# Kernel tuning notes

Measured on AMD Instinct MI355X. Metric: run time of the kernel, lower is better.

## Reference

```python
import jax, jax.numpy as jnp
import numpy as np

EPS = 1e-5
M = 8          # num_modules
NUM_LAYERS = 4


def gumbel_softmax(logits, u, tau):
    g = -jnp.log(-jnp.log(jnp.clip(u, 1e-10, 1.0 - 1e-7)))
    return jax.nn.softmax((logits + g) / tau, axis=-1)


def batchnorm(x, gamma, beta):
    # training-mode BN over batch axis 0; x: [B, ...], gamma/beta broadcast over trailing dims
    mean = jnp.mean(x, axis=0, keepdims=True)
    var = jnp.mean(jnp.square(x - mean), axis=0, keepdims=True)  # biased var, as torch BN
    return (x - mean) * jax.lax.rsqrt(var + EPS) * gamma + beta


def setup_inputs() -> dict:
    key = jax.random.key(0)
    ks = jax.random.split(key, 32)
    B = 16384
    d = {}
    d['x'] = jax.random.normal(ks[0], (B, 128), jnp.float32)
    d['embedding_input'] = jax.random.normal(ks[1], (B, 128), jnp.float32)
    d['u_sel'] = jax.random.uniform(ks[2], (B, NUM_LAYERS - 1, M, M), jnp.float32)
    d['u_final'] = jax.random.uniform(ks[3], (B, M), jnp.float32)
    shapes = [('base_W0', (128, 400)), ('base_b0', (400,)), ('base_W1', (400, 256)), ('base_b1', (256,)),
              ('em_W0', (128, 400)), ('em_b0', (400,)),
              ('gat_W0', (400, 256)), ('gat_b0', (256,)), ('gat_W1', (256, 256)), ('gat_b1', (256,)),
              ('sel_W', (3, 256, 64)), ('sel_b', (3, 64)), ('selF_W', (256, 8)), ('selF_b', (8,)),
              ('cond_W', (3, 64, 256)), ('cond_b', (3, 256)),
              ('mod_W', (8, 256, 256)), ('mod_b', (8, 256)),
              ('last_W', (256, 18)), ('last_b', (18,))]
    for i, (name, sh) in enumerate(shapes):
        fan_in = sh[-2] if len(sh) >= 2 else sh[-1]
        d[name] = jax.random.normal(ks[4 + i], sh, jnp.float32) / np.sqrt(fan_in)
    d['bn1_g'] = jnp.ones((8, 256), jnp.float32)
    d['bn1_b'] = jnp.zeros((8, 256), jnp.float32)
    d['bn2_g'] = jnp.ones((8, 256), jnp.float32)
    d['bn2_b'] = jnp.zeros((8, 256), jnp.float32)
    return d


def forward(x, embedding_input, u_sel, u_final,
            base_W0, base_b0, base_W1, base_b1, em_W0, em_b0,
            gat_W0, gat_b0, gat_W1, gat_b1,
            sel_W, sel_b, selF_W, selF_b, cond_W, cond_b,
            mod_W, mod_b, bn1_g, bn1_b, bn2_g, bn2_b, last_W, last_b):
    relu = jax.nn.relu
    # base MLP (last activation is identity)
    h = relu(x @ base_W0 + base_b0)
    out = h @ base_W1 + base_b1                       # [B, 256]
    # embedding base (single layer, identity last activation)
    emb = embedding_input @ em_W0 + em_b0             # [B, 400]
    # gating fcs: activation THEN fc, per source loop
    emb = relu(emb) @ gat_W0 + gat_b0
    emb = relu(emb) @ gat_W1 + gat_b1                 # [B, 256]

    # routing logits (stochastic branch, tau = select_temp = 1.0)
    select_input = relu(emb)
    gsels = []
    for i in range(NUM_LAYERS - 1):
        logit = jnp.tanh(select_input @ sel_W[i] + sel_b[i])       # [B, 64]
        sraw = logit.reshape(logit.shape[0], M, M)                  # [B, M, M]
        gsels.append(gumbel_softmax(sraw, u_sel[:, i], 1.0))
        select_input = relu((logit @ cond_W[i] + cond_b[i]) * emb)
    final_select = gumbel_softmax(select_input @ selF_W + selF_b, u_final, 1.0)  # [B, M]
    # selects were insert(0, ...)'d in torch -> consumed in reversed order
    selects = gsels[::-1]

    # layer-0 expert modules: BN -> Linear -> BN (only layers[0] is used in forward)
    mean = jnp.mean(out, axis=0, keepdims=True)
    var = jnp.mean(jnp.square(out - mean), axis=0, keepdims=True)
    xhat = (out - mean) * jax.lax.rsqrt(var + EPS)                  # shared normalization
    t = xhat[:, None, :] * bn1_g + bn1_b                            # [B, M, 256] per-module affine
    h = jnp.einsum('bmd,mdh->bmh', t, mod_W) + mod_b                # [B, M, 256]
    prev = batchnorm(h, bn2_g, bn2_b)                               # [B, M, 256]

    # cascade: weighted combination + relu per layer
    for l in range(NUM_LAYERS - 1):
        prev = relu(jnp.einsum('bmk,bkh->bmh', selects[l], prev))
    out = jnp.einsum('bm,bmh->bh', final_select, prev)              # [B, 256]
    return out @ last_W + last_b                                    # [B, 18]


def reference(x, embedding_input, u_sel, u_final,
              base_W0, base_b0, base_W1, base_b1, em_W0, em_b0,
              gat_W0, gat_b0, gat_W1, gat_b1,
              sel_W, sel_b, selF_W, selF_b, cond_W, cond_b,
              mod_W, mod_b, bn1_g, bn1_b, bn2_g, bn2_b, last_W, last_b):
    return forward(x, embedding_input, u_sel, u_final,
                   base_W0, base_b0, base_W1, base_b1, em_W0, em_b0,
                   gat_W0, gat_b0, gat_W1, gat_b1,
                   sel_W, sel_b, selF_W, selF_b, cond_W, cond_b,
                   mod_W, mod_b, bn1_g, bn1_b, bn2_g, bn2_b, last_W, last_b)
```

## Files before the change

### kernel.cpp

```cpp
#include <hip/hip_runtime.h>
#include <math.h>


#define EPI_NONE  0
#define EPI_RELU  1
#define EPI_TANH  2
#define EPI_COND  3
#define EPI_STATS 4

typedef short bf16x8 __attribute__((ext_vector_type(8)));
typedef float f32x4 __attribute__((ext_vector_type(4)));

__device__ __forceinline__ unsigned short f2bf(float f) {
  unsigned u = __float_as_uint(f);
  u += 0x7fffu + ((u >> 16) & 1u);
  return (unsigned short)(u >> 16);
}
__device__ __forceinline__ float bf2f(unsigned short h) {
  return __uint_as_float(((unsigned)h) << 16);
}
__device__ __forceinline__ void gload_lds16(const void* g, void* l) {
  __builtin_amdgcn_global_load_lds(
      (const __attribute__((address_space(1))) unsigned int*)g,
      (__attribute__((address_space(3))) unsigned int*)l, 16, 0, 0);
}
__device__ __forceinline__ bf16x8 relu_bf8(bf16x8 v) {
  bf16x8 r;
  #pragma unroll
  for (int j = 0; j < 8; ++j) r[j] = v[j] > 0 ? v[j] : (short)0;
  return r;
}

__global__ __launch_bounds__(256) void prep_all(
    const float* __restrict__ x, const float* __restrict__ embi,
    const float* __restrict__ base_W0, const float* __restrict__ em_W0,
    const float* __restrict__ base_W1, const float* __restrict__ gat_W0,
    const float* __restrict__ gat_W1, const float* __restrict__ sel_W,
    const float* __restrict__ cond_W, const float* __restrict__ last_W,
    unsigned short* __restrict__ x_bf, unsigned short* __restrict__ e_bf,
    unsigned short* __restrict__ W0t, unsigned short* __restrict__ emW0t,
    unsigned short* __restrict__ W1t, unsigned short* __restrict__ g0t,
    unsigned short* __restrict__ g1t, unsigned short* __restrict__ selWt,
    unsigned short* __restrict__ condWt, unsigned short* __restrict__ lastWt,
    float* __restrict__ stats)
{
  __shared__ float t[32][33];
  int bid = blockIdx.x;
  const int tid = threadIdx.x;

  if (bid < 4096) {
    const float* src = bid < 2048 ? x : embi;
    unsigned short* dst = bid < 2048 ? x_bf : e_bf;
    const int i = ((bid & 2047) * 256 + tid) * 4;
    const float4 v = *reinterpret_cast<const float4*>(&src[i]);
    ushort4 o;
    o.x = f2bf(v.x); o.y = f2bf(v.y); o.z = f2bf(v.z); o.w = f2bf(v.w);
    *reinterpret_cast<ushort4*>(&dst[i]) = o;
    return;
  }
  bid -= 4096;

  const int tx = tid & 31, ty = tid >> 5;

  if (bid < 496) {
    const float* src; unsigned short* dst; int K, N, KP, gx, local;
    if (bid < 64)       { src = base_W0; dst = W0t;   K = 128; N = 400; KP = 128; gx = 4;  local = bid; }
    else if (bid < 128) { src = em_W0;   dst = emW0t; K = 128; N = 400; KP = 128; gx = 4;  local = bid - 64; }
    else if (bid < 232) { src = base_W1; dst = W1t;   K = 400; N = 256; KP = 416; gx = 13; local = bid - 128; }
    else if (bid < 336) { src = gat_W0;  dst = g0t;   K = 400; N = 256; KP = 416; gx = 13; local = bid - 232; }
    else if (bid < 400) { src = gat_W1;  dst = g1t;   K = 256; N = 256; KP = 256; gx = 8;  local = bid - 336; }
    else if (bid < 448) {
      const int i = (bid - 400) / 16;
      src = sel_W + i * 16384; dst = selWt + i * 16384;
      K = 256; N = 64; KP = 256; gx = 8; local = (bid - 400) % 16;
    } else {
      const int i = (bid - 448) / 16;
      src = cond_W + i * 16384; dst = condWt + i * 16384;
      K = 64; N = 256; KP = 64; gx = 2; local = (bid - 448) % 16;
    }
    const int k0 = (local % gx) * 32, n0 = (local / gx) * 32;
    #pragma unroll
    for (int p = 0; p < 4; ++p) {
      const int k = k0 + ty + p * 8;
      t[ty + p * 8][tx] = (k < K && n0 + tx < N) ? src[(size_t)k * N + n0 + tx] : 0.f;
    }
    __syncthreads();
    #pragma unroll
    for (int p = 0; p < 4; ++p) {
      const int n = n0 + ty + p * 8;
      dst[(size_t)n * KP + k0 + tx] = f2bf(t[tx][ty + p * 8]);
    }
    return;
  }
  bid -= 496;

  if (bid < 8) {
    const int k0 = bid * 32;
    #pragma unroll
    for (int p = 0; p < 4; ++p)
      t[ty + p * 8][tx] = (tx < 18) ? last_W[(size_t)(k0 + ty + p * 8) * 18 + tx] : 0.f;
    __syncthreads();
    #pragma unroll
    for (int p = 0; p < 4; ++p) {
      const int n = ty + p * 8;
      lastWt[(size_t)n * 256 + k0 + tx] = f2bf(t[tx][n]);
      lastWt[(size_t)(n + 32) * 256 + k0 + tx] = 0;
    }
    return;
  }

  for (int i = tid; i < 4608; i += 256) stats[i] = 0.f;
}

template<int BN, int WM, int WN, int EPI, bool RELU_A>
__global__ __launch_bounds__(256) void gemm_bf16(
    const unsigned short* __restrict__ A, int AS,
    const unsigned short* __restrict__ Wt, const float* __restrict__ bias,
    unsigned short* __restrict__ C, int CS, int Nreal, int NP, int K,
    const unsigned short* __restrict__ emb,
    float* __restrict__ sum, float* __restrict__ sumsq,
    const unsigned short* A2, const unsigned short* W2,
    const float* bias_b, unsigned short* C2)
{
  constexpr int FRAG_M = 128 / WM / 16;
  constexpr int FRAG_N = BN / WN / 16;
  __shared__ unsigned short As[128 * 32];
  __shared__ unsigned short Bs[BN * 32];
  const unsigned short* Ap = (blockIdx.z == 0) ? A : A2;
  const unsigned short* Wp = (blockIdx.z == 0) ? Wt : W2;
  const float* bp = (blockIdx.z == 0) ? bias : bias_b;
  unsigned short* Cp = (blockIdx.z == 0) ? C : C2;
  const int row0 = blockIdx.y * 128;
  const int n0 = blockIdx.x * BN;
  const int tid = threadIdx.x;
  const int wid = tid >> 6, lane = tid & 63;
  const int wr = wid / WN, wc = wid % WN;
  const int arow = tid >> 2;
  const int kcol = (tid & 3) * 8;
  const int lr = lane & 15, lk = (lane >> 4) * 8;
  const int lrow = (lane >> 4) * 4;

  f32x4 acc[FRAG_M][FRAG_N] = {};
  for (int k0 = 0; k0 < K; k0 += 32) {
    gload_lds16(Ap + (size_t)(row0 + arow) * AS + k0 + kcol, (char*)As + tid * 16);
    gload_lds16(Ap + (size_t)(row0 + 64 + arow) * AS + k0 + kcol, (char*)As + 4096 + tid * 16);
    gload_lds16(Wp + (size_t)(n0 + arow) * K + k0 + kcol, (char*)Bs + tid * 16);
    if constexpr (BN == 128)
      gload_lds16(Wp + (size_t)(n0 + 64 + arow) * K + k0 + kcol, (char*)Bs + 4096 + tid * 16);
    __syncthreads();
    bf16x8 a[FRAG_M], b[FRAG_N];
    #pragma unroll
    for (int i = 0; i < FRAG_M; ++i) {
      a[i] = *reinterpret_cast<const bf16x8*>(&As[(wr * (128 / WM) + i * 16 + lr) * 32 + lk]);
      if (RELU_A) a[i] = relu_bf8(a[i]);
    }
    #pragma unroll
    for (int j = 0; j < FRAG_N; ++j)
      b[j] = *reinterpret_cast<const bf16x8*>(&Bs[(wc * (BN / WN) + j * 16 + lr) * 32 + lk]);
    #pragma unroll
    for (int i = 0; i < FRAG_M; ++i)
      #pragma unroll
      for (int j = 0; j < FRAG_N; ++j)
        acc[i][j] = __builtin_amdgcn_mfma_f32_16x16x32_bf16(a[i], b[j], acc[i][j], 0, 0, 0);
    __syncthreads();
  }
  #pragma unroll
  for (int j = 0; j < FRAG_N; ++j) {
    const int col = n0 + wc * (BN / WN) + j * 16 + lr;
    if (col >= NP) continue;
    const bool real = col < Nreal;
    const float bv = real ? bp[col] : 0.f;
    float s = 0.f, q = 0.f;
    #pragma unroll
    for (int i = 0; i < FRAG_M; ++i) {
      #pragma unroll
      for (int r = 0; r < 4; ++r) {
        const int row = row0 + wr * (128 / WM) + i * 16 + lrow + r;
        float v = acc[i][j][r] + bv;
        if (EPI == EPI_RELU) v = fmaxf(v, 0.f);
        if (EPI == EPI_TANH) v = tanhf(v);
        if (EPI == EPI_COND) { v *= bf2f(emb[(size_t)row * 256 + col]); v = fmaxf(v, 0.f); }
        if (!real) v = 0.f;
        const unsigned short hv = f2bf(v);
        Cp[(size_t)row * CS + col] = hv;
        if (EPI == EPI_STATS) {
          const float vr = bf2f(hv);
          s += vr;
          q = fmaf(vr, vr, q);
        }
      }
    }
    if (EPI == EPI_STATS) {
      s += __shfl_xor(s, 16); s += __shfl_xor(s, 32);
      q += __shfl_xor(q, 16); q += __shfl_xor(q, 32);
      if (lane < 16) {
        atomicAdd(&sum[col], s);
        atomicAdd(&sumsq[col], q);
      }
    }
  }
}

__global__ __launch_bounds__(256) void gemm_mod_frag(
    const unsigned short* __restrict__ Abf,
    const unsigned short* __restrict__ Wt2,
    const float* __restrict__ bias2,
    unsigned short* __restrict__ H,
    float* __restrict__ sum, float* __restrict__ sumsq)
{
  __shared__ unsigned short Cs[128 * 136];
  const int tid = threadIdx.x;
  const int wid = tid >> 6, lane = tid & 63;
  const int wr = wid >> 1, wc = wid & 1;
  const int lr = lane & 15, hi = lane >> 4;
  const int m = blockIdx.x >> 1, half = blockIdx.x & 1;
  const int row0 = blockIdx.y * 128;

  const unsigned short* Wbase =
      Wt2 + (size_t)(m * 16 + half * 8 + wc * 4) * 8 * 512 + lane * 8;
  const unsigned short* Abase = Abf + (size_t)(row0 + wr * 64 + lr) * 256 + hi * 8;

  f32x4 acc[4][4] = {};
  #pragma unroll 2
  for (int ks = 0; ks < 8; ++ks) {
    bf16x8 a[4], b[4];
    #pragma unroll
    for (int i = 0; i < 4; ++i)
      a[i] = *reinterpret_cast<const bf16x8*>(Abase + (size_t)i * 16 * 256 + ks * 32);
    #pragma unroll
    for (int j = 0; j < 4; ++j)
      b[j] = *reinterpret_cast<const bf16x8*>(Wbase + ((size_t)j * 8 + ks) * 512);
    #pragma unroll
    for (int i = 0; i < 4; ++i)
      #pragma unroll
      for (int j = 0; j < 4; ++j)
        acc[i][j] = __builtin_amdgcn_mfma_f32_16x16x32_bf16(a[i], b[j], acc[i][j], 0, 0, 0);
  }

  #pragma unroll
  for (int j = 0; j < 4; ++j) {
    const int J = half * 8 + wc * 4 + j;
    const int gc = m * 256 + J * 16 + lr;
    const float bv = bias2[gc];
    float s = 0.f, q = 0.f;
    #pragma unroll
    for (int i = 0; i < 4; ++i) {
      #pragma unroll
      for (int r = 0; r < 4; ++r) {
        const unsigned short hv = f2bf(acc[i][j][r] + bv);
        Cs[(wr * 64 + i * 16 + hi * 4 + r) * 136 + wc * 64 + j * 16 + lr] = hv;
        const float vr = bf2f(hv);
        s += vr;
        q = fmaf(vr, vr, q);
      }
    }
    s += __shfl_xor(s, 16); s += __shfl_xor(s, 32);
    q += __shfl_xor(q, 16); q += __shfl_xor(q, 32);
    if (lane < 16) {
      atomicAdd(&sum[gc], s);
      atomicAdd(&sumsq[gc], q);
    }
  }
  __syncthreads();
  const int colbase = m * 256 + half * 128;
  #pragma unroll
  for (int pass = 0; pass < 2; ++pass) {
    const int row = pass * 64 + (tid >> 2);
    const int qc = (tid & 3) * 32;
    #pragma unroll
    for (int v = 0; v < 4; ++v) {
      const uint4 d = *reinterpret_cast<const uint4*>(&Cs[row * 136 + qc + v * 8]);
      *reinterpret_cast<uint4*>(&H[(size_t)(row0 + row) * 2048 + colbase + qc + v * 8]) = d;
    }
  }
}

__global__ void gumbel8(const unsigned short* __restrict__ logit, const float* __restrict__ u,
                        float* __restrict__ out, int u_off, int u_stride)
{
  const int idx = blockIdx.x * 256 + threadIdx.x;
  const int b = idx >> 3, m = idx & 7;
  const unsigned short* lp = logit + (size_t)b * 64 + m * 8;
  const float* up = u + (size_t)b * u_stride + u_off + m * 8;
  float v[8];
  #pragma unroll
  for (int j = 0; j < 8; ++j) {
    const float uu = fminf(fmaxf(up[j], 1e-10f), 0.9999999f);
    v[j] = bf2f(lp[j]) - logf(-logf(uu));
  }
  float mx = v[0];
  #pragma unroll
  for (int j = 1; j < 8; ++j) mx = fmaxf(mx, v[j]);
  float s = 0.f;
  #pragma unroll
  for (int j = 0; j < 8; ++j) { v[j] = expf(v[j] - mx); s += v[j]; }
  const float inv = 1.f / s;
  float* op = out + (size_t)b * 64 + m * 8;
  #pragma unroll
  for (int j = 0; j < 8; ++j) op[j] = v[j] * inv;
}

__global__ void final_select_k(const unsigned short* __restrict__ si, const float* __restrict__ Wf,
                               const float* __restrict__ bias, const float* __restrict__ u,
                               float* __restrict__ fs)
{
  const int idx = blockIdx.x * 256 + threadIdx.x;
  const int b = idx >> 3, j = idx & 7;
  const unsigned short* sp = si + (size_t)b * 256;
  float acc = bias[j];
  for (int k = 0; k < 256; ++k) acc = fmaf(bf2f(sp[k]), Wf[k * 8 + j], acc);
  const float uu = fminf(fmaxf(u[(size_t)b * 8 + j], 1e-10f), 0.9999999f);
  float v = acc - logf(-logf(uu));
  float mx = v;
  #pragma unroll
  for (int d = 1; d < 8; d <<= 1) mx = fmaxf(mx, __shfl_xor(mx, d, 8));
  float e = expf(v - mx);
  float s = e;
  #pragma unroll
  for (int d = 1; d < 8; d <<= 1) s += __shfl_xor(s, d, 8);
  fs[(size_t)b * 8 + j] = e / s;
}

__global__ __launch_bounds__(256) void fold_modw_all(
    const float* __restrict__ W, const float* __restrict__ g1,
    const float* __restrict__ b1, const float* __restrict__ modb,
    const float* __restrict__ sum1, const float* __restrict__ sumsq1,
    unsigned short* __restrict__ Wt, float* __restrict__ bias2)
{
  const float invB = 1.f / 16384.f;
  if (blockIdx.z == 8) {
    if (blockIdx.y != 0) return;
    const int m = blockIdx.x, h = threadIdx.x;
    float acc = modb[m * 256 + h];
    for (int d = 0; d < 256; ++d) {
      const float mean = sum1[d] * invB;
      const float var = sumsq1[d] * invB - mean * mean;
      const float r = rsqrtf(var + 1e-5f);
      const float c = b1[m * 256 + d] - mean * r * g1[m * 256 + d];
      acc = fmaf(c, W[((size_t)m * 256 + d) * 256 + h], acc);
    }
    bias2[m * 256 + h] = acc;
    return;
  }
  __shared__ float t[32][33];
  const int m = blockIdx.z, d0 = blockIdx.y * 32, h0 = blockIdx.x * 32;
  const int tx = threadIdx.x & 31, ty = threadIdx.x >> 5;
  #pragma unroll
  for (int p = 0; p < 4; ++p) {
    const int d = d0 + ty + p * 8;
    const float mean = sum1[d] * invB;
    const float var = sumsq1[d] * invB - mean * mean;
    const float r = rsqrtf(var + 1e-5f);
    t[ty + p * 8][tx] = W[((size_t)m * 256 + d) * 256 + h0 + tx] * r * g1[m * 256 + d];
  }
  __syncthreads();
  #pragma unroll
  for (int p = 0; p < 4; ++p) {
    const int h = h0 + ty + p * 8;
    Wt[((size_t)m * 256 + h) * 256 + d0 + tx] = f2bf(t[tx][ty + p * 8]);
  }
}

__global__ __launch_bounds__(256) void reshuffle_w(
    const unsigned short* __restrict__ modWt, unsigned short* __restrict__ Wt2)
{
  const int idx = blockIdx.x * 256 + threadIdx.x;
  const int ks = idx & 7, col = (idx >> 3) & 255, m = idx >> 11;
  const unsigned short* src = modWt + ((size_t)m * 256 + col) * 256 + ks * 32;
  unsigned short* dst = Wt2 + (size_t)((m * 16 + (col >> 4)) * 8 + ks) * 512 + (col & 15) * 8;
  #pragma unroll
  for (int h2 = 0; h2 < 4; ++h2)
    *reinterpret_cast<uint4*>(dst + h2 * 128) = *reinterpret_cast<const uint4*>(src + h2 * 8);
}

__global__ void finalize_bn2(const float* __restrict__ sum, const float* __restrict__ sumsq,
                             const float* __restrict__ g, const float* __restrict__ b,
                             float* __restrict__ scale, float* __restrict__ shift)
{
  const int i = blockIdx.x * 256 + threadIdx.x;
  const float invB = 1.f / 16384.f;
  const float m = sum[i] * invB;
  const float v = sumsq[i] * invB - m * m;
  const float r = rsqrtf(v + 1e-5f);
  const float sc = r * g[i];
  scale[i] = sc;
  shift[i] = b[i] - m * sc;
}

__global__ __launch_bounds__(256) void final_cascade(
    const unsigned short* __restrict__ H, const float* __restrict__ scale2,
    const float* __restrict__ shift2, const float* __restrict__ gs0,
    const float* __restrict__ gs1, const float* __restrict__ gs2,
    const float* __restrict__ fs, unsigned short* __restrict__ ovec)
{
  const int wave = threadIdx.x >> 6, lane = threadIdx.x & 63;
  const int b = __builtin_amdgcn_readfirstlane(blockIdx.x * 4 + wave);
  const int c0 = lane << 2;

  float prev[8][4];
  #pragma unroll
  for (int m = 0; m < 8; ++m) {
    const int gc = m * 256 + c0;
    const ushort4 h = *reinterpret_cast<const ushort4*>(&H[(size_t)b * 2048 + gc]);
    const float4 sc = *reinterpret_cast<const float4*>(&scale2[gc]);
    const float4 sh = *reinterpret_cast<const float4*>(&shift2[gc]);
    prev[m][0] = bf2f(h.x) * sc.x + sh.x;
    prev[m][1] = bf2f(h.y) * sc.y + sh.y;
    prev[m][2] = bf2f(h.z) * sc.z + sh.z;
    prev[m][3] = bf2f(h.w) * sc.w + sh.w;
  }

  const float* sel0 = gs2 + (size_t)b * 64;
  const float* sel1 = gs1 + (size_t)b * 64;
  const float* sel2 = gs0 + (size_t)b * 64;
  #pragma unroll
  for (int l = 0; l < 3; ++l) {
    const float* sp = (l == 0) ? sel0 : (l == 1) ? sel1 : sel2;
    float nw[8][4];
    #pragma unroll
    for (int m = 0; m < 8; ++m) {
      float a0 = 0.f, a1 = 0.f, a2 = 0.f, a3 = 0.f;
      #pragma unroll
      for (int k = 0; k < 8; ++k) {
        const float s = sp[m * 8 + k];
        a0 = fmaf(s, prev[k][0], a0);
        a1 = fmaf(s, prev[k][1], a1);
        a2 = fmaf(s, prev[k][2], a2);
        a3 = fmaf(s, prev[k][3], a3);
      }
      nw[m][0] = fmaxf(a0, 0.f); nw[m][1] = fmaxf(a1, 0.f);
      nw[m][2] = fmaxf(a2, 0.f); nw[m][3] = fmaxf(a3, 0.f);
    }
    #pragma unroll
    for (int m = 0; m < 8; ++m)
      #pragma unroll
      for (int c = 0; c < 4; ++c)
        prev[m][c] = nw[m][c];
  }

  const float* fp = fs + (size_t)b * 8;
  float ov[4] = {0.f, 0.f, 0.f, 0.f};
  #pragma unroll
  for (int m = 0; m < 8; ++m) {
    const float s = fp[m];
    ov[0] = fmaf(s, prev[m][0], ov[0]);
    ov[1] = fmaf(s, prev[m][1], ov[1]);
    ov[2] = fmaf(s, prev[m][2], ov[2]);
    ov[3] = fmaf(s, prev[m][3], ov[3]);
  }
  ushort4 o;
  o.x = f2bf(ov[0]); o.y = f2bf(ov[1]); o.z = f2bf(ov[2]); o.w = f2bf(ov[3]);
  *reinterpret_cast<ushort4*>(&ovec[(size_t)b * 256 + c0]) = o;
}

__global__ __launch_bounds__(256) void gemm_last(
    const unsigned short* __restrict__ A, const unsigned short* __restrict__ Wt,
    const float* __restrict__ bias, float* __restrict__ out)
{
  __shared__ unsigned short As[128 * 32];
  __shared__ unsigned short Bs[64 * 32];
  const int row0 = blockIdx.y * 128;
  const int tid = threadIdx.x;
  const int wid = tid >> 6, lane = tid & 63;
  const int arow = tid >> 2;
  const int kcol = (tid & 3) * 8;
  const int lr = lane & 15, lk = (lane >> 4) * 8;
  const int lrow = (lane >> 4) * 4;

  f32x4 acc[2][4] = {};
  for (int k0 = 0; k0 < 256; k0 += 32) {
    gload_lds16(A + (size_t)(row0 + arow) * 256 + k0 + kcol, (char*)As + tid * 16);
    gload_lds16(A + (size_t)(row0 + 64 + arow) * 256 + k0 + kcol, (char*)As + 4096 + tid * 16);
    gload_lds16(Wt + (size_t)arow * 256 + k0 + kcol, (char*)Bs + tid * 16);
    __syncthreads();
    bf16x8 a[2], b[4];
    #pragma unroll
    for (int i = 0; i < 2; ++i)
      a[i] = *reinterpret_cast<const bf16x8*>(&As[(wid * 32 + i * 16 + lr) * 32 + lk]);
    #pragma unroll
    for (int j = 0; j < 4; ++j)
      b[j] = *reinterpret_cast<const bf16x8*>(&Bs[(j * 16 + lr) * 32 + lk]);
    #pragma unroll
    for (int i = 0; i < 2; ++i)
      #pragma unroll
      for (int j = 0; j < 4; ++j)
        acc[i][j] = __builtin_amdgcn_mfma_f32_16x16x32_bf16(a[i], b[j], acc[i][j], 0, 0, 0);
    __syncthreads();
  }
  #pragma unroll
  for (int j = 0; j < 2; ++j) {
    const int col = j * 16 + lr;
    if (col >= 18) continue;
    const float bv = bias[col];
    #pragma unroll
    for (int i = 0; i < 2; ++i) {
      #pragma unroll
      for (int r = 0; r < 4; ++r) {
        const int row = row0 + wid * 32 + i * 16 + lrow + r;
        out[(size_t)row * 18 + col] = acc[i][j][r] + bv;
      }
    }
  }
}

extern "C" void kernel_launch(void* const* d_in, const int* in_sizes, int n_in,
                              void* d_out, int out_size, void* d_ws, size_t ws_size,
                              hipStream_t stream)
{
  (void)in_sizes; (void)n_in; (void)out_size; (void)ws_size;
  const float* x       = (const float*)d_in[0];
  const float* embi    = (const float*)d_in[1];
  const float* u_sel   = (const float*)d_in[2];
  const float* u_fin   = (const float*)d_in[3];
  const float* base_W0 = (const float*)d_in[4];
  const float* base_b0 = (const float*)d_in[5];
  const float* base_W1 = (const float*)d_in[6];
  const float* base_b1 = (const float*)d_in[7];
  const float* em_W0   = (const float*)d_in[8];
  const float* em_b0   = (const float*)d_in[9];
  const float* gat_W0  = (const float*)d_in[10];
  const float* gat_b0  = (const float*)d_in[11];
  const float* gat_W1  = (const float*)d_in[12];
  const float* gat_b1  = (const float*)d_in[13];
  const float* sel_W   = (const float*)d_in[14];
  const float* sel_b   = (const float*)d_in[15];
  const float* selF_W  = (const float*)d_in[16];
  const float* selF_b  = (const float*)d_in[17];
  const float* cond_W  = (const float*)d_in[18];
  const float* cond_b  = (const float*)d_in[19];
  const float* mod_W   = (const float*)d_in[20];
  const float* mod_b   = (const float*)d_in[21];
  const float* last_W  = (const float*)d_in[22];
  const float* last_b  = (const float*)d_in[23];
  const float* bn1_g   = (const float*)d_in[24];
  const float* bn1_b   = (const float*)d_in[25];
  const float* bn2_g   = (const float*)d_in[26];
  const float* bn2_b   = (const float*)d_in[27];

  char* WSB = (char*)d_ws;
  unsigned short* h_big    = (unsigned short*)(WSB + 0);
  unsigned short* h1e      = (unsigned short*)(WSB + 67108864);
  unsigned short* ovec_bf  = (unsigned short*)(WSB + 67108864);
  unsigned short* h1       = (unsigned short*)(WSB + 81000448);
  unsigned short* x_bf     = (unsigned short*)(WSB + 94631936);
  unsigned short* e_bf     = (unsigned short*)(WSB + 98826240);
  unsigned short* emb_bf   = (unsigned short*)(WSB + 103020544);
  unsigned short* si_bf    = (unsigned short*)(WSB + 111409152);
  unsigned short* out_bf   = (unsigned short*)(WSB + 119797760);
  unsigned short* logit_bf = (unsigned short*)(WSB + 128186368);
  float* gs0   = (float*)(WSB + 130283520);
  float* gs1   = (float*)(WSB + 134477824);
  float* gs2   = (float*)(WSB + 138672128);
  float* bufFs = (float*)(WSB + 142866432);
  unsigned short* W0t   = (unsigned short*)(WSB + 143390720);
  unsigned short* emW0t = (unsigned short*)(WSB + 143521792);
  unsigned short* W1t   = (unsigned short*)(WSB + 143652864);
  unsigned short* g0t   = (unsigned short*)(WSB + 143865856);
  unsigned short* g1t   = (unsigned short*)(WSB + 144078848);
  unsigned short* selWt = (unsigned short*)(WSB + 144209920);
  unsigned short* condWt= (unsigned short*)(WSB + 144308224);
  unsigned short* modWt = (unsigned short*)(WSB + 144406528);
  unsigned short* Wt2   = (unsigned short*)(WSB + 145455104);
  float* bias2  = (float*)(WSB + 146503680);
  float* stats  = (float*)(WSB + 146511872);
  unsigned short* lastWt = (unsigned short*)(WSB + 146530304);
  float* scale2 = (float*)(WSB + 146563072);
  float* shift2 = (float*)(WSB + 146571264);
  float* sum1   = stats;        float* sumsq1 = stats + 256;
  float* sum2   = stats + 512;  float* sumsq2 = stats + 2560;

  const dim3 blk(256);
  prep_all<<<dim3(4601), blk, 0, stream>>>(
      x, embi, base_W0, em_W0, base_W1, gat_W0, gat_W1, sel_W, cond_W, last_W,
      x_bf, e_bf, W0t, emW0t, W1t, g0t, g1t, selWt, condWt, lastWt, stats);

  gemm_bf16<128, 2, 2, EPI_RELU, false><<<dim3(4, 128, 2), blk, 0, stream>>>(
      x_bf, 128, W0t, base_b0, h1, 416, 400, 416, 128, nullptr, nullptr, nullptr,
      e_bf, emW0t, em_b0, h1e);
  gemm_bf16<64, 4, 1, EPI_STATS, false><<<dim3(4, 128), blk, 0, stream>>>(
      h1, 416, W1t, base_b1, out_bf, 256, 256, 256, 416, nullptr, sum1, sumsq1,
      nullptr, nullptr, nullptr, nullptr);
  gemm_bf16<64, 4, 1, EPI_RELU, false><<<dim3(4, 128), blk, 0, stream>>>(
      h1e, 416, g0t, gat_b0, si_bf, 256, 256, 256, 416, nullptr, nullptr, nullptr,
      nullptr, nullptr, nullptr, nullptr);
  gemm_bf16<64, 4, 1, EPI_NONE, false><<<dim3(4, 128), blk, 0, stream>>>(
      si_bf, 256, g1t, gat_b1, emb_bf, 256, 256, 256, 256, nullptr, nullptr, nullptr,
      nullptr, nullptr, nullptr, nullptr);
  float* gs[3] = {gs0, gs1, gs2};
  for (int i = 0; i < 3; ++i) {
    if (i == 0)
      gemm_bf16<64, 4, 1, EPI_TANH, true><<<dim3(1, 128), blk, 0, stream>>>(
          emb_bf, 256, selWt, sel_b, logit_bf, 64, 64, 64, 256, nullptr, nullptr, nullptr,
          nullptr, nullptr, nullptr, nullptr);
    else
      gemm_bf16<64, 4, 1, EPI_TANH, false><<<dim3(1, 128), blk, 0, stream>>>(
          si_bf, 256, selWt + i * 16384, sel_b + i * 64, logit_bf, 64, 64, 64, 256,
          nullptr, nullptr, nullptr, nullptr, nullptr, nullptr, nullptr);
    gumbel8<<<dim3(512), blk, 0, stream>>>(logit_bf, u_sel, gs[i], i * 64, 192);
    gemm_bf16<64, 4, 1, EPI_COND, false><<<dim3(4, 128), blk, 0, stream>>>(
        logit_bf, 64, condWt + i * 16384, cond_b + i * 256, si_bf, 256, 256, 256, 64,
        emb_bf, nullptr, nullptr, nullptr, nullptr, nullptr, nullptr);
  }
  final_select_k<<<dim3(512), blk, 0, stream>>>(si_bf, selF_W, selF_b, u_fin, bufFs);
  fold_modw_all<<<dim3(8, 8, 9), blk, 0, stream>>>(
      mod_W, bn1_g, bn1_b, mod_b, sum1, sumsq1, modWt, bias2);
  reshuffle_w<<<dim3(64), blk, 0, stream>>>(modWt, Wt2);
  gemm_mod_frag<<<dim3(16, 128), blk, 0, stream>>>(
      out_bf, Wt2, bias2, h_big, sum2, sumsq2);
  finalize_bn2<<<dim3(8), blk, 0, stream>>>(sum2, sumsq2, bn2_g, bn2_b, scale2, shift2);
  final_cascade<<<dim3(4096), blk, 0, stream>>>(
      h_big, scale2, shift2, gs0, gs1, gs2, bufFs, ovec_bf);
  gemm_last<<<dim3(1, 128), blk, 0, stream>>>(ovec_bf, lastWt, last_b, (float*)d_out);
}
```

Measured before the change: 288.9 us.

## Fuse input conversion into first GEMM, fuse select pipeline, replace mod GEMM

The first GEMM now reads the fp32 inputs directly and converts them to bf16 while staging into LDS, so the separate conversion pass and its intermediate buffers are gone. Each selection layer's logits GEMM, tanh, Gumbel-softmax and conditioning GEMM are merged into one kernel that keeps the logits in LDS, replacing three launches per layer. The fragment-layout module GEMM and its weight reshuffle kernel are replaced by a plain LDS-tiled GEMM with a swizzled block order and direct global stores. The risks are that the fused select kernel runs only 128 blocks with a heavy per-block workload, and that the new module GEMM may perform worse than the pre-reshuffled direct-load version.

```diff
diff --git a/kernel.cpp b/kernel.cpp
--- a/kernel.cpp
+++ b/kernel.cpp
@@ -1,12 +1,6 @@
 #include <hip/hip_runtime.h>
 #include <math.h>
 
-
-#define EPI_NONE  0
-#define EPI_RELU  1
-#define EPI_TANH  2
-#define EPI_COND  3
-#define EPI_STATS 4
 
 typedef short bf16x8 __attribute__((ext_vector_type(8)));
 typedef float f32x4 __attribute__((ext_vector_type(4)));
@@ -19,6 +13,9 @@
 __device__ __forceinline__ float bf2f(unsigned short h) {
   return __uint_as_float(((unsigned)h) << 16);
 }
+__device__ __forceinline__ unsigned pack2(float a, float b) {
+  return ((unsigned)f2bf(b) << 16) | f2bf(a);
+}
 __device__ __forceinline__ void gload_lds16(const void* g, void* l) {
   __builtin_amdgcn_global_load_lds(
       (const __attribute__((address_space(1))) unsigned int*)g,
@@ -31,13 +28,15 @@
   return r;
 }
 
+#define EPI_NONE  0
+#define EPI_RELU  1
+#define EPI_STATS 4
+
 __global__ __launch_bounds__(256) void prep_all(
-    const float* __restrict__ x, const float* __restrict__ embi,
     const float* __restrict__ base_W0, const float* __restrict__ em_W0,
     const float* __restrict__ base_W1, const float* __restrict__ gat_W0,
     const float* __restrict__ gat_W1, const float* __restrict__ sel_W,
     const float* __restrict__ cond_W, const float* __restrict__ last_W,
-    unsigned short* __restrict__ x_bf, unsigned short* __restrict__ e_bf,
     unsigned short* __restrict__ W0t, unsigned short* __restrict__ emW0t,
     unsigned short* __restrict__ W1t, unsigned short* __restrict__ g0t,
     unsigned short* __restrict__ g1t, unsigned short* __restrict__ selWt,
@@ -47,19 +46,6 @@
   __shared__ float t[32][33];
   int bid = blockIdx.x;
   const int tid = threadIdx.x;
-
-  if (bid < 4096) {
-    const float* src = bid < 2048 ? x : embi;
-    unsigned short* dst = bid < 2048 ? x_bf : e_bf;
-    const int i = ((bid & 2047) * 256 + tid) * 4;
-    const float4 v = *reinterpret_cast<const float4*>(&src[i]);
-    ushort4 o;
-    o.x = f2bf(v.x); o.y = f2bf(v.y); o.z = f2bf(v.z); o.w = f2bf(v.w);
-    *reinterpret_cast<ushort4*>(&dst[i]) = o;
-    return;
-  }
-  bid -= 4096;
-
   const int tx = tid & 31, ty = tid >> 5;
 
   if (bid < 496) {
@@ -112,24 +98,89 @@
   for (int i = tid; i < 4608; i += 256) stats[i] = 0.f;
 }
 
+__global__ __launch_bounds__(256) void gemm_w0(
+    const float* __restrict__ Ax, const float* __restrict__ Ae,
+    const unsigned short* __restrict__ Wx, const unsigned short* __restrict__ We,
+    const float* __restrict__ bx, const float* __restrict__ be,
+    unsigned short* __restrict__ Cx, unsigned short* __restrict__ Ce)
+{
+  __shared__ unsigned short As[128 * 32];
+  __shared__ unsigned short Bs[128 * 32];
+  const float* Ap = blockIdx.z ? Ae : Ax;
+  const unsigned short* Wp = blockIdx.z ? We : Wx;
+  const float* bp = blockIdx.z ? be : bx;
+  unsigned short* Cp = blockIdx.z ? Ce : Cx;
+  const int row0 = blockIdx.y * 128;
+  const int n0 = blockIdx.x * 128;
+  const int tid = threadIdx.x;
+  const int wid = tid >> 6, lane = tid & 63;
+  const int wr = wid >> 1, wc = wid & 1;
+  const int arow = tid >> 2, kcol = (tid & 3) * 8;
+  const int lr = lane & 15, lk = (lane >> 4) * 8;
+  const int lrow = (lane >> 4) * 4;
+
+  f32x4 acc[4][4] = {};
+  for (int k0 = 0; k0 < 128; k0 += 32) {
+    {
+      const float4* s1 = reinterpret_cast<const float4*>(
+          Ap + (size_t)(row0 + arow) * 128 + k0 + kcol);
+      uint4 w1 = {pack2(s1[0].x, s1[0].y), pack2(s1[0].z, s1[0].w),
+                  pack2(s1[1].x, s1[1].y), pack2(s1[1].z, s1[1].w)};
+      *reinterpret_cast<uint4*>(&As[arow * 32 + kcol]) = w1;
+      const float4* s2 = reinterpret_cast<const float4*>(
+          Ap + (size_t)(row0 + 64 + arow) * 128 + k0 + kcol);
+      uint4 w2 = {pack2(s2[0].x, s2[0].y), pack2(s2[0].z, s2[0].w),
+                  pack2(s2[1].x, s2[1].y), pack2(s2[1].z, s2[1].w)};
+      *reinterpret_cast<uint4*>(&As[(64 + arow) * 32 + kcol]) = w2;
+    }
+    gload_lds16(Wp + (size_t)(n0 + arow) * 128 + k0 + kcol, (char*)Bs + tid * 16);
+    gload_lds16(Wp + (size_t)(n0 + 64 + arow) * 128 + k0 + kcol,
+                (char*)Bs + 4096 + tid * 16);
+    __syncthreads();
+    bf16x8 a[4], b[4];
+    #pragma unroll
+    for (int i = 0; i < 4; ++i)
+      a[i] = *reinterpret_cast<const bf16x8*>(&As[(wr * 64 + i * 16 + lr) * 32 + lk]);
+    #pragma unroll
+    for (int j = 0; j < 4; ++j)
+      b[j] = *reinterpret_cast<const bf16x8*>(&Bs[(wc * 64 + j * 16 + lr) * 32 + lk]);
+    #pragma unroll
+    for (int i = 0; i < 4; ++i)
+      #pragma unroll
+      for (int j = 0; j < 4; ++j)
+        acc[i][j] = __builtin_amdgcn_mfma_f32_16x16x32_bf16(a[i], b[j], acc[i][j], 0, 0, 0);
+    __syncthreads();
+  }
+  #pragma unroll
+  for (int j = 0; j < 4; ++j) {
+    const int col = n0 + wc * 64 + j * 16 + lr;
+    if (col >= 416) continue;
+    const bool real = col < 400;
+    const float bv = real ? bp[col] : 0.f;
+    #pragma unroll
+    for (int i = 0; i < 4; ++i) {
+      #pragma unroll
+      for (int r = 0; r < 4; ++r) {
+        const int row = row0 + wr * 64 + i * 16 + lrow + r;
+        float v = real ? fmaxf(acc[i][j][r] + bv, 0.f) : 0.f;
+        Cp[(size_t)row * 416 + col] = f2bf(v);
+      }
+    }
+  }
+}
+
 template<int BN, int WM, int WN, int EPI, bool RELU_A>
 __global__ __launch_bounds__(256) void gemm_bf16(
     const unsigned short* __restrict__ A, int AS,
     const unsigned short* __restrict__ Wt, const float* __restrict__ bias,
     unsigned short* __restrict__ C, int CS, int Nreal, int NP, int K,
     const unsigned short* __restrict__ emb,
-    float* __restrict__ sum, float* __restrict__ sumsq,
-    const unsigned short* A2, const unsigned short* W2,
-    const float* bias_b, unsigned short* C2)
+    float* __restrict__ sum, float* __restrict__ sumsq)
 {
   constexpr int FRAG_M = 128 / WM / 16;
   constexpr int FRAG_N = BN / WN / 16;
   __shared__ unsigned short As[128 * 32];
   __shared__ unsigned short Bs[BN * 32];
-  const unsigned short* Ap = (blockIdx.z == 0) ? A : A2;
-  const unsigned short* Wp = (blockIdx.z == 0) ? Wt : W2;
-  const float* bp = (blockIdx.z == 0) ? bias : bias_b;
-  unsigned short* Cp = (blockIdx.z == 0) ? C : C2;
   const int row0 = blockIdx.y * 128;
   const int n0 = blockIdx.x * BN;
   const int tid = threadIdx.x;
@@ -142,11 +193,11 @@
 
   f32x4 acc[FRAG_M][FRAG_N] = {};
   for (int k0 = 0; k0 < K; k0 += 32) {
-    gload_lds16(Ap + (size_t)(row0 + arow) * AS + k0 + kcol, (char*)As + tid * 16);
-    gload_lds16(Ap + (size_t)(row0 + 64 + arow) * AS + k0 + kcol, (char*)As + 4096 + tid * 16);
-    gload_lds16(Wp + (size_t)(n0 + arow) * K + k0 + kcol, (char*)Bs + tid * 16);
+    gload_lds16(A + (size_t)(row0 + arow) * AS + k0 + kcol, (char*)As + tid * 16);
+    gload_lds16(A + (size_t)(row0 + 64 + arow) * AS + k0 + kcol, (char*)As + 4096 + tid * 16);
+    gload_lds16(Wt + (size_t)(n0 + arow) * K + k0 + kcol, (char*)Bs + tid * 16);
     if constexpr (BN == 128)
-      gload_lds16(Wp + (size_t)(n0 + 64 + arow) * K + k0 + kcol, (char*)Bs + 4096 + tid * 16);
+      gload_lds16(Wt + (size_t)(n0 + 64 + arow) * K + k0 + kcol, (char*)Bs + 4096 + tid * 16);
     __syncthreads();
     bf16x8 a[FRAG_M], b[FRAG_N];
     #pragma unroll
@@ -169,7 +220,7 @@
     const int col = n0 + wc * (BN / WN) + j * 16 + lr;
     if (col >= NP) continue;
     const bool real = col < Nreal;
-    const float bv = real ? bp[col] : 0.f;
+    const float bv = real ? bias[col] : 0.f;
     float s = 0.f, q = 0.f;
     #pragma unroll
     for (int i = 0; i < FRAG_M; ++i) {
@@ -178,11 +229,9 @@
         const int row = row0 + wr * (128 / WM) + i * 16 + lrow + r;
         float v = acc[i][j][r] + bv;
         if (EPI == EPI_RELU) v = fmaxf(v, 0.f);
-        if (EPI == EPI_TANH) v = tanhf(v);
-        if (EPI == EPI_COND) { v *= bf2f(emb[(size_t)row * 256 + col]); v = fmaxf(v, 0.f); }
         if (!real) v = 0.f;
         const unsigned short hv = f2bf(v);
-        Cp[(size_t)row * CS + col] = hv;
+        C[(size_t)row * CS + col] = hv;
         if (EPI == EPI_STATS) {
           const float vr = bf2f(hv);
           s += vr;
@@ -201,54 +250,59 @@
   }
 }
 
-__global__ __launch_bounds__(256) void gemm_mod_frag(
-    const unsigned short* __restrict__ Abf,
-    const unsigned short* __restrict__ Wt2,
-    const float* __restrict__ bias2,
-    unsigned short* __restrict__ H,
+__global__ __launch_bounds__(256) void gemm_mod(
+    const unsigned short* __restrict__ A,
+    const unsigned short* __restrict__ Wt,
+    const float* __restrict__ bias, unsigned short* __restrict__ C,
     float* __restrict__ sum, float* __restrict__ sumsq)
 {
-  __shared__ unsigned short Cs[128 * 136];
+  __shared__ unsigned short As[128 * 32];
+  __shared__ unsigned short Bs[128 * 32];
+  const int lin = blockIdx.x;
+  const int swz = (lin & 7) * 256 + (lin >> 3);
+  const int row0 = (swz >> 4) * 128;
+  const int n0 = (swz & 15) * 128;
   const int tid = threadIdx.x;
   const int wid = tid >> 6, lane = tid & 63;
   const int wr = wid >> 1, wc = wid & 1;
-  const int lr = lane & 15, hi = lane >> 4;
-  const int m = blockIdx.x >> 1, half = blockIdx.x & 1;
-  const int row0 = blockIdx.y * 128;
-
-  const unsigned short* Wbase =
-      Wt2 + (size_t)(m * 16 + half * 8 + wc * 4) * 8 * 512 + lane * 8;
-  const unsigned short* Abase = Abf + (size_t)(row0 + wr * 64 + lr) * 256 + hi * 8;
+  const int arow = tid >> 2;
+  const int kcol = (tid & 3) * 8;
+  const int lr = lane & 15, lk = (lane >> 4) * 8;
+  const int lrow = (lane >> 4) * 4;
 
   f32x4 acc[4][4] = {};
-  #pragma unroll 2
-  for (int ks = 0; ks < 8; ++ks) {
+  for (int k0 = 0; k0 < 256; k0 += 32) {
+    gload_lds16(A + (size_t)(row0 + arow) * 256 + k0 + kcol, (char*)As + tid * 16);
+    gload_lds16(A + (size_t)(row0 + 64 + arow) * 256 + k0 + kcol, (char*)As + 4096 + tid * 16);
+    gload_lds16(Wt + (size_t)(n0 + arow) * 256 + k0 + kcol, (char*)Bs + tid * 16);
+    gload_lds16(Wt + (size_t)(n0 + 64 + arow) * 256 + k0 + kcol, (char*)Bs + 4096 + tid * 16);
+    __syncthreads();
     bf16x8 a[4], b[4];
     #pragma unroll
     for (int i = 0; i < 4; ++i)
-      a[i] = *reinterpret_cast<const bf16x8*>(Abase + (size_t)i * 16 * 256 + ks * 32);
+      a[i] = *reinterpret_cast<const bf16x8*>(&As[(wr * 64 + i * 16 + lr) * 32 + lk]);
     #pragma unroll
     for (int j = 0; j < 4; ++j)
-      b[j] = *reinterpret_cast<const bf16x8*>(Wbase + ((size_t)j * 8 + ks) * 512);
+      b[j] = *reinterpret_cast<const bf16x8*>(&Bs[(wc * 64 + j * 16 + lr) * 32 + lk]);
     #pragma unroll
     for (int i = 0; i < 4; ++i)
       #pragma unroll
       for (int j = 0; j < 4; ++j)
         acc[i][j] = __builtin_amdgcn_mfma_f32_16x16x32_bf16(a[i], b[j], acc[i][j], 0, 0, 0);
-  }
-
+    __syncthreads();
+  }
   #pragma unroll
   for (int j = 0; j < 4; ++j) {
-    const int J = half * 8 + wc * 4 + j;
-    const int gc = m * 256 + J * 16 + lr;
-    const float bv = bias2[gc];
+    const int col = n0 + wc * 64 + j * 16 + lr;
+    const float bv = bias[col];
     float s = 0.f, q = 0.f;
     #pragma unroll
     for (int i = 0; i < 4; ++i) {
       #pragma unroll
       for (int r = 0; r < 4; ++r) {
+        const int row = row0 + wr * 64 + i * 16 + lrow + r;
         const unsigned short hv = f2bf(acc[i][j][r] + bv);
-        Cs[(wr * 64 + i * 16 + hi * 4 + r) * 136 + wc * 64 + j * 16 + lr] = hv;
+        C[(size_t)row * 2048 + col] = hv;
         const float vr = bf2f(hv);
         s += vr;
         q = fmaf(vr, vr, q);
@@ -257,47 +311,128 @@
     s += __shfl_xor(s, 16); s += __shfl_xor(s, 32);
     q += __shfl_xor(q, 16); q += __shfl_xor(q, 32);
     if (lane < 16) {
-      atomicAdd(&sum[gc], s);
-      atomicAdd(&sumsq[gc], q);
+      atomicAdd(&sum[col], s);
+      atomicAdd(&sumsq[col], q);
+    }
+  }
+}
+
+template<bool RELU_A>
+__global__ __launch_bounds__(256) void fused_select(
+    const unsigned short* __restrict__ A, const unsigned short* __restrict__ selWt,
+    const float* __restrict__ selb, const unsigned short* __restrict__ condWt,
+    const float* __restrict__ condb, const unsigned short* __restrict__ emb,
+    const float* __restrict__ u, int u_off,
+    float* __restrict__ gs, unsigned short* __restrict__ siout)
+{
+  __shared__ unsigned short As[128 * 32];
+  __shared__ unsigned short Bs[64 * 32];
+  __shared__ unsigned short Ls[128 * 72];
+  const int tid = threadIdx.x;
+  const int wid = tid >> 6, lane = tid & 63;
+  const int lr = lane & 15, hi = lane >> 4;
+  const int lk = hi * 8;
+  const int row0 = blockIdx.x * 128;
+  const int arow = tid >> 2, kcol = (tid & 3) * 8;
+
+  {
+    f32x4 acc[2][4] = {};
+    for (int k0 = 0; k0 < 256; k0 += 32) {
+      gload_lds16(A + (size_t)(row0 + arow) * 256 + k0 + kcol, (char*)As + tid * 16);
+      gload_lds16(A + (size_t)(row0 + 64 + arow) * 256 + k0 + kcol, (char*)As + 4096 + tid * 16);
+      gload_lds16(selWt + (size_t)arow * 256 + k0 + kcol, (char*)Bs + tid * 16);
+      __syncthreads();
+      bf16x8 a[2], b[4];
+      #pragma unroll
+      for (int i = 0; i < 2; ++i) {
+        a[i] = *reinterpret_cast<const bf16x8*>(&As[(wid * 32 + i * 16 + lr) * 32 + lk]);
+        if (RELU_A) a[i] = relu_bf8(a[i]);
+      }
+      #pragma unroll
+      for (int j = 0; j < 4; ++j)
+        b[j] = *reinterpret_cast<const bf16x8*>(&Bs[(j * 16 + lr) * 32 + lk]);
+      #pragma unroll
+      for (int i = 0; i < 2; ++i)
+        #pragma unroll
+        for (int j = 0; j < 4; ++j)
+          acc[i][j] = __builtin_amdgcn_mfma_f32_16x16x32_bf16(a[i], b[j], acc[i][j], 0, 0, 0);
+      __syncthreads();
+    }
+    #pragma unroll
+    for (int j = 0; j < 4; ++j) {
+      const int col = j * 16 + lr;
+      const float bv = selb[col];
+      #pragma unroll
+      for (int i = 0; i < 2; ++i)
+        #pragma unroll
+        for (int r = 0; r < 4; ++r) {
+          const int row = wid * 32 + i * 16 + hi * 4 + r;
+          Ls[row * 72 + col] = f2bf(tanhf(acc[i][j][r] + bv));
+        }
     }
   }
   __syncthreads();
-  const int colbase = m * 256 + half * 128;
-  #pragma unroll
-  for (int pass = 0; pass < 2; ++pass) {
-    const int row = pass * 64 + (tid >> 2);
-    const int qc = (tid & 3) * 32;
-    #pragma unroll
-    for (int v = 0; v < 4; ++v) {
-      const uint4 d = *reinterpret_cast<const uint4*>(&Cs[row * 136 + qc + v * 8]);
-      *reinterpret_cast<uint4*>(&H[(size_t)(row0 + row) * 2048 + colbase + qc + v * 8]) = d;
-    }
-  }
-}
-
-__global__ void gumbel8(const unsigned short* __restrict__ logit, const float* __restrict__ u,
-                        float* __restrict__ out, int u_off, int u_stride)
-{
-  const int idx = blockIdx.x * 256 + threadIdx.x;
-  const int b = idx >> 3, m = idx & 7;
-  const unsigned short* lp = logit + (size_t)b * 64 + m * 8;
-  const float* up = u + (size_t)b * u_stride + u_off + m * 8;
-  float v[8];
-  #pragma unroll
-  for (int j = 0; j < 8; ++j) {
-    const float uu = fminf(fmaxf(up[j], 1e-10f), 0.9999999f);
-    v[j] = bf2f(lp[j]) - logf(-logf(uu));
-  }
-  float mx = v[0];
-  #pragma unroll
-  for (int j = 1; j < 8; ++j) mx = fmaxf(mx, v[j]);
-  float s = 0.f;
-  #pragma unroll
-  for (int j = 0; j < 8; ++j) { v[j] = expf(v[j] - mx); s += v[j]; }
-  const float inv = 1.f / s;
-  float* op = out + (size_t)b * 64 + m * 8;
-  #pragma unroll
-  for (int j = 0; j < 8; ++j) op[j] = v[j] * inv;
+
+  #pragma unroll
+  for (int p = 0; p < 4; ++p) {
+    const int pair = p * 256 + tid;
+    const int bl = pair >> 3, mm = pair & 7;
+    const int bg = row0 + bl;
+    float v[8];
+    #pragma unroll
+    for (int jj = 0; jj < 8; ++jj) v[jj] = bf2f(Ls[bl * 72 + mm * 8 + jj]);
+    const float* up = u + (size_t)bg * 192 + u_off + mm * 8;
+    #pragma unroll
+    for (int jj = 0; jj < 8; ++jj) {
+      const float uu = fminf(fmaxf(up[jj], 1e-10f), 0.9999999f);
+      v[jj] -= logf(-logf(uu));
+    }
+    float mx = v[0];
+    #pragma unroll
+    for (int jj = 1; jj < 8; ++jj) mx = fmaxf(mx, v[jj]);
+    float s = 0.f;
+    #pragma unroll
+    for (int jj = 0; jj < 8; ++jj) { v[jj] = expf(v[jj] - mx); s += v[jj]; }
+    const float inv = 1.f / s;
+    float* op = gs + (size_t)bg * 64 + mm * 8;
+    #pragma unroll
+    for (int jj = 0; jj < 8; ++jj) op[jj] = v[jj] * inv;
+  }
+
+  {
+    const int wr2 = wid >> 1, wc2 = wid & 1;
+    f32x4 acc2[4][8] = {};
+    #pragma unroll
+    for (int kq = 0; kq < 2; ++kq) {
+      const int k0 = kq * 32;
+      bf16x8 a2[4];
+      #pragma unroll
+      for (int i = 0; i < 4; ++i)
+        a2[i] = *reinterpret_cast<const bf16x8*>(
+            &Ls[(wr2 * 64 + i * 16 + lr) * 72 + k0 + hi * 8]);
+      #pragma unroll
+      for (int j = 0; j < 8; ++j) {
+        const bf16x8 b2 = *reinterpret_cast<const bf16x8*>(
+            condWt + (size_t)(wc2 * 128 + j * 16 + lr) * 64 + k0 + hi * 8);
+        #pragma unroll
+        for (int i = 0; i < 4; ++i)
+          acc2[i][j] = __builtin_amdgcn_mfma_f32_16x16x32_bf16(a2[i], b2, acc2[i][j], 0, 0, 0);
+      }
+    }
+    #pragma unroll
+    for (int j = 0; j < 8; ++j) {
+      const int col = wc2 * 128 + j * 16 + lr;
+      const float bv = condb[col];
+      #pragma unroll
+      for (int i = 0; i < 4; ++i)
+        #pragma unroll
+        for (int r = 0; r < 4; ++r) {
+          const int row = row0 + wr2 * 64 + i * 16 + hi * 4 + r;
+          float vv = (acc2[i][j][r] + bv) * bf2f(emb[(size_t)row * 256 + col]);
+          siout[(size_t)row * 256 + col] = f2bf(fmaxf(vv, 0.f));
+        }
+    }
+  }
 }
 
 __global__ void final_select_k(const unsigned short* __restrict__ si, const float* __restrict__ Wf,
@@ -359,18 +494,6 @@
     const int h = h0 + ty + p * 8;
     Wt[((size_t)m * 256 + h) * 256 + d0 + tx] = f2bf(t[tx][ty + p * 8]);
   }
-}
-
-__global__ __launch_bounds__(256) void reshuffle_w(
-    const unsigned short* __restrict__ modWt, unsigned short* __restrict__ Wt2)
-{
-  const int idx = blockIdx.x * 256 + threadIdx.x;
-  const int ks = idx & 7, col = (idx >> 3) & 255, m = idx >> 11;
-  const unsigned short* src = modWt + ((size_t)m * 256 + col) * 256 + ks * 32;
-  unsigned short* dst = Wt2 + (size_t)((m * 16 + (col >> 4)) * 8 + ks) * 512 + (col & 15) * 8;
-  #pragma unroll
-  for (int h2 = 0; h2 < 4; ++h2)
-    *reinterpret_cast<uint4*>(dst + h2 * 128) = *reinterpret_cast<const uint4*>(src + h2 * 8);
 }
 
 __global__ void finalize_bn2(const float* __restrict__ sum, const float* __restrict__ sumsq,
@@ -542,12 +665,9 @@
   unsigned short* h1e      = (unsigned short*)(WSB + 67108864);
   unsigned short* ovec_bf  = (unsigned short*)(WSB + 67108864);
   unsigned short* h1       = (unsigned short*)(WSB + 81000448);
-  unsigned short* x_bf     = (unsigned short*)(WSB + 94631936);
-  unsigned short* e_bf     = (unsigned short*)(WSB + 98826240);
   unsigned short* emb_bf   = (unsigned short*)(WSB + 103020544);
   unsigned short* si_bf    = (unsigned short*)(WSB + 111409152);
   unsigned short* out_bf   = (unsigned short*)(WSB + 119797760);
-  unsigned short* logit_bf = (unsigned short*)(WSB + 128186368);
   float* gs0   = (float*)(WSB + 130283520);
   float* gs1   = (float*)(WSB + 134477824);
   float* gs2   = (float*)(WSB + 138672128);
@@ -560,7 +680,6 @@
   unsigned short* selWt = (unsigned short*)(WSB + 144209920);
   unsigned short* condWt= (unsigned short*)(WSB + 144308224);
   unsigned short* modWt = (unsigned short*)(WSB + 144406528);
-  unsigned short* Wt2   = (unsigned short*)(WSB + 145455104);
   float* bias2  = (float*)(WSB + 146503680);
   float* stats  = (float*)(WSB + 146511872);
   unsigned short* lastWt = (unsigned short*)(WSB + 146530304);
@@ -570,43 +689,30 @@
   float* sum2   = stats + 512;  float* sumsq2 = stats + 2560;
 
   const dim3 blk(256);
-  prep_all<<<dim3(4601), blk, 0, stream>>>(
-      x, embi, base_W0, em_W0, base_W1, gat_W0, gat_W1, sel_W, cond_W, last_W,
-      x_bf, e_bf, W0t, emW0t, W1t, g0t, g1t, selWt, condWt, lastWt, stats);
-
-  gemm_bf16<128, 2, 2, EPI_RELU, false><<<dim3(4, 128, 2), blk, 0, stream>>>(
-      x_bf, 128, W0t, base_b0, h1, 416, 400, 416, 128, nullptr, nullptr, nullptr,
-      e_bf, emW0t, em_b0, h1e);
+  prep_all<<<dim3(505), blk, 0, stream>>>(
+      base_W0, em_W0, base_W1, gat_W0, gat_W1, sel_W, cond_W, last_W,
+      W0t, emW0t, W1t, g0t, g1t, selWt, condWt, lastWt, stats);
+
+  gemm_w0<<<dim3(4, 128, 2), blk, 0, stream>>>(
+      x, embi, W0t, emW0t, base_b0, em_b0, h1, h1e);
   gemm_bf16<64, 4, 1, EPI_STATS, false><<<dim3(4, 128), blk, 0, stream>>>(
-      h1, 416, W1t, base_b1, out_bf, 256, 256, 256, 416, nullptr, sum1, sumsq1,
-      nullptr, nullptr, nullptr, nullptr);
+      h1, 416, W1t, base_b1, out_bf, 256, 256, 256, 416, nullptr, sum1, sumsq1);
   gemm_bf16<64, 4, 1, EPI_RELU, false><<<dim3(4, 128), blk, 0, stream>>>(
-      h1e, 416, g0t, gat_b0, si_bf, 256, 256, 256, 416, nullptr, nullptr, nullptr,
-      nullptr, nullptr, nullptr, nullptr);
+      h1e, 416, g0t, gat_b0, si_bf, 256, 256, 256, 416, nullptr, nullptr, nullptr);
   gemm_bf16<64, 4, 1, EPI_NONE, false><<<dim3(4, 128), blk, 0, stream>>>(
-      si_bf, 256, g1t, gat_b1, emb_bf, 256, 256, 256, 256, nullptr, nullptr, nullptr,
-      nullptr, nullptr, nullptr, nullptr);
-  float* gs[3] = {gs0, gs1, gs2};
-  for (int i = 0; i < 3; ++i) {
-    if (i == 0)
-      gemm_bf16<64, 4, 1, EPI_TANH, true><<<dim3(1, 128), blk, 0, stream>>>(
-          emb_bf, 256, selWt, sel_b, logit_bf, 64, 64, 64, 256, nullptr, nullptr, nullptr,
-          nullptr, nullptr, nullptr, nullptr);
-    else
-      gemm_bf16<64, 4, 1, EPI_TANH, false><<<dim3(1, 128), blk, 0, stream>>>(
-          si_bf, 256, selWt + i * 16384, sel_b + i * 64, logit_bf, 64, 64, 64, 256,
-          nullptr, nullptr, nullptr, nullptr, nullptr, nullptr, nullptr);
-    gumbel8<<<dim3(512), blk, 0, stream>>>(logit_bf, u_sel, gs[i], i * 64, 192);
-    gemm_bf16<64, 4, 1, EPI_COND, false><<<dim3(4, 128), blk, 0, stream>>>(
-        logit_bf, 64, condWt + i * 16384, cond_b + i * 256, si_bf, 256, 256, 256, 64,
-        emb_bf, nullptr, nullptr, nullptr, nullptr, nullptr, nullptr);
-  }
+      si_bf, 256, g1t, gat_b1, emb_bf, 256, 256, 256, 256, nullptr, nullptr, nullptr);
+  fused_select<true><<<dim3(128), blk, 0, stream>>>(
+      emb_bf, selWt, sel_b, condWt, cond_b, emb_bf, u_sel, 0, gs0, si_bf);
+  fused_select<false><<<dim3(128), blk, 0, stream>>>(
+      si_bf, selWt + 16384, sel_b + 64, condWt + 16384, cond_b + 256, emb_bf,
+      u_sel, 64, gs1, si_bf);
+  fused_select<false><<<dim3(128), blk, 0, stream>>>(
+      si_bf, selWt + 32768, sel_b + 128, condWt + 32768, cond_b + 512, emb_bf,
+      u_sel, 128, gs2, si_bf);
   final_select_k<<<dim3(512), blk, 0, stream>>>(si_bf, selF_W, selF_b, u_fin, bufFs);
   fold_modw_all<<<dim3(8, 8, 9), blk, 0, stream>>>(
       mod_W, bn1_g, bn1_b, mod_b, sum1, sumsq1, modWt, bias2);
-  reshuffle_w<<<dim3(64), blk, 0, stream>>>(modWt, Wt2);
-  gemm_mod_frag<<<dim3(16, 128), blk, 0, stream>>>(
-      out_bf, Wt2, bias2, h_big, sum2, sumsq2);
+  gemm_mod<<<dim3(2048), blk, 0, stream>>>(out_bf, modWt, bias2, h_big, sum2, sumsq2);
   finalize_bn2<<<dim3(8), blk, 0, stream>>>(sum2, sumsq2, bn2_g, bn2_b, scale2, shift2);
   final_cascade<<<dim3(4096), blk, 0, stream>>>(
       h_big, scale2, shift2, gs0, gs1, gs2, bufFs, ovec_bf);
```

New measurement: 256.6 us. 1.13x faster.
